# Optimization experiments

Hardware: AMD Instinct MI355X
Metric: run time of the kernel (lower is better)

The kernel has to match this reference:

```python
import jax, jax.numpy as jnp
import numpy as np

# T-MAC weight-only quantized linear, mathematically-equivalent reference.
# Weights: ternary {-1,0,1} via per-tensor scale s_w = 1/mean|W| (pesudo_tmac_weight_quant,
# force_per_tensor=True). Dequant scale = 1/s_w.
# Activations: the LUT preprocessing quantizes per act_group_size=64 group to uint8 with
# per-group LUT_Scales/LUT_Biases; equivalent math is symmetric int8 per-group quantization.
# qgemm_lut accumulates LUT entries indexed by weight bits == qW @ x_hat, then applies scales.

ACT_GROUP = 64  # op_config.act_group_size


def setup_inputs() -> dict:
    key = jax.random.key(0)
    k1, k2 = jax.random.split(key)
    N, M, K = 8, 8192, 8192
    x = jax.random.normal(k1, (N, K), dtype=jnp.float32)
    weight = jax.random.normal(k2, (M, K), dtype=jnp.float32) * 0.02
    return {"x": x, "weight": weight}


def reference(x, weight):
    M, K = weight.shape
    N = x.shape[0]
    # --- weight ternary quantization (per-tensor) ---
    s_w = 1.0 / jnp.clip(jnp.mean(jnp.abs(weight)), 1e-5, None)
    qW = jnp.clip(jnp.round(weight * s_w), -1.0, 1.0)  # [M, K] in {-1,0,1}
    w_deq = 1.0 / s_w  # per-tensor dequant scale (weight_scales)
    # --- activation per-group int8 quantization (LUT precision emulation) ---
    xg = x.reshape(N, K // ACT_GROUP, ACT_GROUP)
    a_scale = jnp.maximum(jnp.max(jnp.abs(xg), axis=-1, keepdims=True) / 127.0, 1e-8)
    x_hat = (jnp.round(xg / a_scale) * a_scale).reshape(N, K)
    # --- lookup-accumulate GEMM == dense GEMM with quantized operands ---
    y = jnp.einsum('nk,mk->nm', x_hat, qW) * w_deq  # [N, M]
    return y.astype(x.dtype)
```

## Files before the change

### kernel.cpp

```cpp
#include <hip/hip_runtime.h>
#include <math.h>

#define K_DIM 8192
#define M_DIM 8192
#define N_DIM 8
#define KC 1024
#define RED_BLOCKS 2048

__global__ __launch_bounds__(256) void k_abssum(const float4* __restrict__ W4,
                                                double* __restrict__ partials,
                                                int n4) {
    int tid = blockIdx.x * blockDim.x + threadIdx.x;
    int stride = gridDim.x * blockDim.x;
    float s0 = 0.f, s1 = 0.f, s2 = 0.f, s3 = 0.f;
    for (int i = tid; i < n4; i += stride) {
        float4 v = W4[i];
        s0 += fabsf(v.x); s1 += fabsf(v.y);
        s2 += fabsf(v.z); s3 += fabsf(v.w);
    }
    float s = (s0 + s1) + (s2 + s3);
    #pragma unroll
    for (int off = 32; off > 0; off >>= 1) s += __shfl_xor(s, off, 64);
    __shared__ float sm[4];
    if ((threadIdx.x & 63) == 0) sm[threadIdx.x >> 6] = s;
    __syncthreads();
    if (threadIdx.x == 0) {
        double t = ((double)sm[0] + (double)sm[1]) +
                   ((double)sm[2] + (double)sm[3]);
        partials[blockIdx.x] = t;
    }
}

__global__ __launch_bounds__(256) void k_final(const double* __restrict__ partials,
                                               int nparts,
                                               float* __restrict__ scal) {
    double s = 0.0;
    for (int i = threadIdx.x; i < nparts; i += 256) s += partials[i];
    #pragma unroll
    for (int off = 32; off > 0; off >>= 1) s += __shfl_xor(s, off, 64);
    __shared__ double sm[4];
    if ((threadIdx.x & 63) == 0) sm[threadIdx.x >> 6] = s;
    __syncthreads();
    if (threadIdx.x == 0) {
        double tot = (sm[0] + sm[1]) + (sm[2] + sm[3]);
        float meanf = (float)(tot / (double)((long long)M_DIM * K_DIM));
        float clipped = fmaxf(meanf, 1e-5f);
        float s_w = 1.0f / clipped;
        float w_deq = 1.0f / s_w;
        scal[0] = s_w;
        scal[1] = w_deq;
    }
}

__global__ __launch_bounds__(256) void k_actq(const float* __restrict__ x,
                                              float* __restrict__ xh) {
    int idx = blockIdx.x * blockDim.x + threadIdx.x;
    float v = x[idx];
    float a = fabsf(v);
    #pragma unroll
    for (int off = 32; off > 0; off >>= 1) a = fmaxf(a, __shfl_xor(a, off, 64));
    float scale = fmaxf(a / 127.0f, 1e-8f);
    float q = rintf(v / scale);
    xh[idx] = q * scale;
}

__device__ __forceinline__ float quant1(float w, float s_w) {
    return fminf(1.0f, fmaxf(-1.0f, rintf(w * s_w)));
}

__global__ __launch_bounds__(256) void k_gemm(const float* __restrict__ W,
                                              const float* __restrict__ xh,
                                              const float* __restrict__ scal,
                                              float* __restrict__ out) {
    __shared__ float lds[N_DIM * KC];
    const float s_w  = scal[0];
    const float w_deq = scal[1];
    const int wave = threadIdx.x >> 6;
    const int lane = threadIdx.x & 63;
    const int m0 = blockIdx.x * 16 + wave * 4;

    const float* Wr0 = W + (size_t)(m0 + 0) * K_DIM;
    const float* Wr1 = W + (size_t)(m0 + 1) * K_DIM;
    const float* Wr2 = W + (size_t)(m0 + 2) * K_DIM;
    const float* Wr3 = W + (size_t)(m0 + 3) * K_DIM;

    float acc[4][8];
    #pragma unroll
    for (int r = 0; r < 4; ++r)
        #pragma unroll
        for (int n = 0; n < 8; ++n) acc[r][n] = 0.0f;

    for (int c0 = 0; c0 < K_DIM; c0 += KC) {
        #pragma unroll
        for (int i = 0; i < 8; ++i) {
            int idx = threadIdx.x + i * 256;
            int n = idx >> 8;
            int kk4 = idx & 255;
            float4 v = *(const float4*)(xh + n * K_DIM + c0 + kk4 * 4);
            *(float4*)(lds + n * KC + kk4 * 4) = v;
        }
        __syncthreads();

        #pragma unroll
        for (int it = 0; it < KC / 256; ++it) {
            const int kk = it * 256 + lane * 4;
            const int k = c0 + kk;
            float4 w0 = *(const float4*)(Wr0 + k);
            float4 w1 = *(const float4*)(Wr1 + k);
            float4 w2 = *(const float4*)(Wr2 + k);
            float4 w3 = *(const float4*)(Wr3 + k);
            float4 xv[8];
            #pragma unroll
            for (int n = 0; n < 8; ++n)
                xv[n] = *(const float4*)(lds + n * KC + kk);

            float4 q0, q1, q2, q3;
            q0.x = quant1(w0.x, s_w); q0.y = quant1(w0.y, s_w);
            q0.z = quant1(w0.z, s_w); q0.w = quant1(w0.w, s_w);
            q1.x = quant1(w1.x, s_w); q1.y = quant1(w1.y, s_w);
            q1.z = quant1(w1.z, s_w); q1.w = quant1(w1.w, s_w);
            q2.x = quant1(w2.x, s_w); q2.y = quant1(w2.y, s_w);
            q2.z = quant1(w2.z, s_w); q2.w = quant1(w2.w, s_w);
            q3.x = quant1(w3.x, s_w); q3.y = quant1(w3.y, s_w);
            q3.z = quant1(w3.z, s_w); q3.w = quant1(w3.w, s_w);

            #pragma unroll
            for (int n = 0; n < 8; ++n) {
                acc[0][n] = fmaf(q0.x, xv[n].x, acc[0][n]);
                acc[0][n] = fmaf(q0.y, xv[n].y, acc[0][n]);
                acc[0][n] = fmaf(q0.z, xv[n].z, acc[0][n]);
                acc[0][n] = fmaf(q0.w, xv[n].w, acc[0][n]);
                acc[1][n] = fmaf(q1.x, xv[n].x, acc[1][n]);
                acc[1][n] = fmaf(q1.y, xv[n].y, acc[1][n]);
                acc[1][n] = fmaf(q1.z, xv[n].z, acc[1][n]);
                acc[1][n] = fmaf(q1.w, xv[n].w, acc[1][n]);
                acc[2][n] = fmaf(q2.x, xv[n].x, acc[2][n]);
                acc[2][n] = fmaf(q2.y, xv[n].y, acc[2][n]);
                acc[2][n] = fmaf(q2.z, xv[n].z, acc[2][n]);
                acc[2][n] = fmaf(q2.w, xv[n].w, acc[2][n]);
                acc[3][n] = fmaf(q3.x, xv[n].x, acc[3][n]);
                acc[3][n] = fmaf(q3.y, xv[n].y, acc[3][n]);
                acc[3][n] = fmaf(q3.z, xv[n].z, acc[3][n]);
                acc[3][n] = fmaf(q3.w, xv[n].w, acc[3][n]);
            }
        }
        __syncthreads();
    }

    #pragma unroll
    for (int r = 0; r < 4; ++r) {
        #pragma unroll
        for (int n = 0; n < 8; ++n) {
            float v = acc[r][n];
            #pragma unroll
            for (int off = 32; off > 0; off >>= 1) v += __shfl_xor(v, off, 64);
            acc[r][n] = v;
        }
    }
    if (lane == 0) {
        #pragma unroll
        for (int r = 0; r < 4; ++r)
            #pragma unroll
            for (int n = 0; n < 8; ++n)
                out[n * M_DIM + (m0 + r)] = w_deq * acc[r][n];
    }
}

extern "C" void kernel_launch(void* const* d_in, const int* in_sizes, int n_in,
                              void* d_out, int out_size, void* d_ws, size_t ws_size,
                              hipStream_t stream) {
    const float* x = (const float*)d_in[0];
    const float* W = (const float*)d_in[1];
    float* out = (float*)d_out;

    double* partials = (double*)d_ws;
    float* scal = (float*)((char*)d_ws + 16384);
    float* xh = (float*)((char*)d_ws + 32768);

    const int n4 = (M_DIM * K_DIM) / 4;

    k_abssum<<<RED_BLOCKS, 256, 0, stream>>>((const float4*)W, partials, n4);
    k_final<<<1, 256, 0, stream>>>(partials, RED_BLOCKS, scal);
    k_actq<<<(N_DIM * K_DIM) / 256, 256, 0, stream>>>(x, xh);
    k_gemm<<<M_DIM / 16, 256, 0, stream>>>(W, xh, scal, out);
}
```

Before: 412.1 us.

## Fuse reductions and activation quant into two kernels, drop LDS staging in GEMM

Merges the four launches into two. The first kernel computes per-block abs-sum partials over contiguous weight chunks and also quantizes the activations. The second kernel has every block redundantly reduce the partials to get the scale, then runs the GEMM reading activations straight from global/L2 instead of staging them in LDS with barriers. This removes two launches and the per-chunk syncs, at the cost of each of the 512 blocks repeating the partials reduction and leaning on cache for the activation reads.

```diff
diff --git a/kernel.cpp b/kernel.cpp
--- a/kernel.cpp
+++ b/kernel.cpp
@@ -4,17 +4,17 @@
 #define K_DIM 8192
 #define M_DIM 8192
 #define N_DIM 8
-#define KC 1024
 #define RED_BLOCKS 2048
 
-__global__ __launch_bounds__(256) void k_abssum(const float4* __restrict__ W4,
-                                                double* __restrict__ partials,
-                                                int n4) {
-    int tid = blockIdx.x * blockDim.x + threadIdx.x;
-    int stride = gridDim.x * blockDim.x;
+__global__ __launch_bounds__(256) void k_pass1(const float4* __restrict__ W4,
+                                               const float* __restrict__ x,
+                                               double* __restrict__ partials,
+                                               float* __restrict__ xh) {
+    const float4* p = W4 + (size_t)blockIdx.x * 8192 + threadIdx.x;
     float s0 = 0.f, s1 = 0.f, s2 = 0.f, s3 = 0.f;
-    for (int i = tid; i < n4; i += stride) {
-        float4 v = W4[i];
+    #pragma unroll 8
+    for (int j = 0; j < 32; ++j) {
+        float4 v = p[(size_t)j * 256];
         s0 += fabsf(v.x); s1 += fabsf(v.y);
         s2 += fabsf(v.z); s3 += fabsf(v.w);
     }
@@ -29,52 +29,41 @@
                    ((double)sm[2] + (double)sm[3]);
         partials[blockIdx.x] = t;
     }
-}
 
-__global__ __launch_bounds__(256) void k_final(const double* __restrict__ partials,
-                                               int nparts,
-                                               float* __restrict__ scal) {
-    double s = 0.0;
-    for (int i = threadIdx.x; i < nparts; i += 256) s += partials[i];
-    #pragma unroll
-    for (int off = 32; off > 0; off >>= 1) s += __shfl_xor(s, off, 64);
-    __shared__ double sm[4];
-    if ((threadIdx.x & 63) == 0) sm[threadIdx.x >> 6] = s;
-    __syncthreads();
-    if (threadIdx.x == 0) {
-        double tot = (sm[0] + sm[1]) + (sm[2] + sm[3]);
-        float meanf = (float)(tot / (double)((long long)M_DIM * K_DIM));
-        float clipped = fmaxf(meanf, 1e-5f);
-        float s_w = 1.0f / clipped;
-        float w_deq = 1.0f / s_w;
-        scal[0] = s_w;
-        scal[1] = w_deq;
+    if (blockIdx.x < (N_DIM * K_DIM) / 256) {
+        int idx = blockIdx.x * 256 + threadIdx.x;
+        float v = x[idx];
+        float a = fabsf(v);
+        #pragma unroll
+        for (int off = 32; off > 0; off >>= 1)
+            a = fmaxf(a, __shfl_xor(a, off, 64));
+        float scale = fmaxf(a / 127.0f, 1e-8f);
+        xh[idx] = rintf(v / scale) * scale;
     }
-}
-
-__global__ __launch_bounds__(256) void k_actq(const float* __restrict__ x,
-                                              float* __restrict__ xh) {
-    int idx = blockIdx.x * blockDim.x + threadIdx.x;
-    float v = x[idx];
-    float a = fabsf(v);
-    #pragma unroll
-    for (int off = 32; off > 0; off >>= 1) a = fmaxf(a, __shfl_xor(a, off, 64));
-    float scale = fmaxf(a / 127.0f, 1e-8f);
-    float q = rintf(v / scale);
-    xh[idx] = q * scale;
 }
 
 __device__ __forceinline__ float quant1(float w, float s_w) {
     return fminf(1.0f, fmaxf(-1.0f, rintf(w * s_w)));
 }
 
-__global__ __launch_bounds__(256) void k_gemm(const float* __restrict__ W,
-                                              const float* __restrict__ xh,
-                                              const float* __restrict__ scal,
-                                              float* __restrict__ out) {
-    __shared__ float lds[N_DIM * KC];
-    const float s_w  = scal[0];
-    const float w_deq = scal[1];
+__global__ __launch_bounds__(256) void k_pass2(const float* __restrict__ W,
+                                               const float* __restrict__ xh,
+                                               const double* __restrict__ partials,
+                                               float* __restrict__ out) {
+    double s = 0.0;
+    #pragma unroll
+    for (int j = 0; j < RED_BLOCKS / 256; ++j)
+        s += partials[threadIdx.x + j * 256];
+    #pragma unroll
+    for (int off = 32; off > 0; off >>= 1) s += __shfl_xor(s, off, 64);
+    __shared__ double sm[4];
+    if ((threadIdx.x & 63) == 0) sm[threadIdx.x >> 6] = s;
+    __syncthreads();
+    const double tot = (sm[0] + sm[1]) + (sm[2] + sm[3]);
+    const float meanf = (float)(tot / (double)((long long)M_DIM * K_DIM));
+    const float s_w = 1.0f / fmaxf(meanf, 1e-5f);
+    const float w_deq = 1.0f / s_w;
+
     const int wave = threadIdx.x >> 6;
     const int lane = threadIdx.x & 63;
     const int m0 = blockIdx.x * 16 + wave * 4;
@@ -90,61 +79,46 @@
         #pragma unroll
         for (int n = 0; n < 8; ++n) acc[r][n] = 0.0f;
 
-    for (int c0 = 0; c0 < K_DIM; c0 += KC) {
+    #pragma unroll 2
+    for (int k = lane * 4; k < K_DIM; k += 256) {
+        float4 w0 = *(const float4*)(Wr0 + k);
+        float4 w1 = *(const float4*)(Wr1 + k);
+        float4 w2 = *(const float4*)(Wr2 + k);
+        float4 w3 = *(const float4*)(Wr3 + k);
+        float4 xv[8];
         #pragma unroll
-        for (int i = 0; i < 8; ++i) {
-            int idx = threadIdx.x + i * 256;
-            int n = idx >> 8;
-            int kk4 = idx & 255;
-            float4 v = *(const float4*)(xh + n * K_DIM + c0 + kk4 * 4);
-            *(float4*)(lds + n * KC + kk4 * 4) = v;
-        }
-        __syncthreads();
+        for (int n = 0; n < 8; ++n)
+            xv[n] = *(const float4*)(xh + n * K_DIM + k);
+
+        float4 q0, q1, q2, q3;
+        q0.x = quant1(w0.x, s_w); q0.y = quant1(w0.y, s_w);
+        q0.z = quant1(w0.z, s_w); q0.w = quant1(w0.w, s_w);
+        q1.x = quant1(w1.x, s_w); q1.y = quant1(w1.y, s_w);
+        q1.z = quant1(w1.z, s_w); q1.w = quant1(w1.w, s_w);
+        q2.x = quant1(w2.x, s_w); q2.y = quant1(w2.y, s_w);
+        q2.z = quant1(w2.z, s_w); q2.w = quant1(w2.w, s_w);
+        q3.x = quant1(w3.x, s_w); q3.y = quant1(w3.y, s_w);
+        q3.z = quant1(w3.z, s_w); q3.w = quant1(w3.w, s_w);
 
         #pragma unroll
-        for (int it = 0; it < KC / 256; ++it) {
-            const int kk = it * 256 + lane * 4;
-            const int k = c0 + kk;
-            float4 w0 = *(const float4*)(Wr0 + k);
-            float4 w1 = *(const float4*)(Wr1 + k);
-            float4 w2 = *(const float4*)(Wr2 + k);
-            float4 w3 = *(const float4*)(Wr3 + k);
-            float4 xv[8];
-            #pragma unroll
-            for (int n = 0; n < 8; ++n)
-                xv[n] = *(const float4*)(lds + n * KC + kk);
-
-            float4 q0, q1, q2, q3;
-            q0.x = quant1(w0.x, s_w); q0.y = quant1(w0.y, s_w);
-            q0.z = quant1(w0.z, s_w); q0.w = quant1(w0.w, s_w);
-            q1.x = quant1(w1.x, s_w); q1.y = quant1(w1.y, s_w);
-            q1.z = quant1(w1.z, s_w); q1.w = quant1(w1.w, s_w);
-            q2.x = quant1(w2.x, s_w); q2.y = quant1(w2.y, s_w);
-            q2.z = quant1(w2.z, s_w); q2.w = quant1(w2.w, s_w);
-            q3.x = quant1(w3.x, s_w); q3.y = quant1(w3.y, s_w);
-            q3.z = quant1(w3.z, s_w); q3.w = quant1(w3.w, s_w);
-
-            #pragma unroll
-            for (int n = 0; n < 8; ++n) {
-                acc[0][n] = fmaf(q0.x, xv[n].x, acc[0][n]);
-                acc[0][n] = fmaf(q0.y, xv[n].y, acc[0][n]);
-                acc[0][n] = fmaf(q0.z, xv[n].z, acc[0][n]);
-                acc[0][n] = fmaf(q0.w, xv[n].w, acc[0][n]);
-                acc[1][n] = fmaf(q1.x, xv[n].x, acc[1][n]);
-                acc[1][n] = fmaf(q1.y, xv[n].y, acc[1][n]);
-                acc[1][n] = fmaf(q1.z, xv[n].z, acc[1][n]);
-                acc[1][n] = fmaf(q1.w, xv[n].w, acc[1][n]);
-                acc[2][n] = fmaf(q2.x, xv[n].x, acc[2][n]);
-                acc[2][n] = fmaf(q2.y, xv[n].y, acc[2][n]);
-                acc[2][n] = fmaf(q2.z, xv[n].z, acc[2][n]);
-                acc[2][n] = fmaf(q2.w, xv[n].w, acc[2][n]);
-                acc[3][n] = fmaf(q3.x, xv[n].x, acc[3][n]);
-                acc[3][n] = fmaf(q3.y, xv[n].y, acc[3][n]);
-                acc[3][n] = fmaf(q3.z, xv[n].z, acc[3][n]);
-                acc[3][n] = fmaf(q3.w, xv[n].w, acc[3][n]);
-            }
+        for (int n = 0; n < 8; ++n) {
+            acc[0][n] = fmaf(q0.x, xv[n].x, acc[0][n]);
+            acc[0][n] = fmaf(q0.y, xv[n].y, acc[0][n]);
+            acc[0][n] = fmaf(q0.z, xv[n].z, acc[0][n]);
+            acc[0][n] = fmaf(q0.w, xv[n].w, acc[0][n]);
+            acc[1][n] = fmaf(q1.x, xv[n].x, acc[1][n]);
+            acc[1][n] = fmaf(q1.y, xv[n].y, acc[1][n]);
+            acc[1][n] = fmaf(q1.z, xv[n].z, acc[1][n]);
+            acc[1][n] = fmaf(q1.w, xv[n].w, acc[1][n]);
+            acc[2][n] = fmaf(q2.x, xv[n].x, acc[2][n]);
+            acc[2][n] = fmaf(q2.y, xv[n].y, acc[2][n]);
+            acc[2][n] = fmaf(q2.z, xv[n].z, acc[2][n]);
+            acc[2][n] = fmaf(q2.w, xv[n].w, acc[2][n]);
+            acc[3][n] = fmaf(q3.x, xv[n].x, acc[3][n]);
+            acc[3][n] = fmaf(q3.y, xv[n].y, acc[3][n]);
+            acc[3][n] = fmaf(q3.z, xv[n].z, acc[3][n]);
+            acc[3][n] = fmaf(q3.w, xv[n].w, acc[3][n]);
         }
-        __syncthreads();
     }
 
     #pragma unroll
@@ -174,13 +148,8 @@
     float* out = (float*)d_out;
 
     double* partials = (double*)d_ws;
-    float* scal = (float*)((char*)d_ws + 16384);
     float* xh = (float*)((char*)d_ws + 32768);
 
-    const int n4 = (M_DIM * K_DIM) / 4;
-
-    k_abssum<<<RED_BLOCKS, 256, 0, stream>>>((const float4*)W, partials, n4);
-    k_final<<<1, 256, 0, stream>>>(partials, RED_BLOCKS, scal);
-    k_actq<<<(N_DIM * K_DIM) / 256, 256, 0, stream>>>(x, xh);
-    k_gemm<<<M_DIM / 16, 256, 0, stream>>>(W, xh, scal, out);
+    k_pass1<<<RED_BLOCKS, 256, 0, stream>>>((const float4*)W, x, partials, xh);
+    k_pass2<<<M_DIM / 16, 256, 0, stream>>>(W, xh, partials, out);
 }
```

Measured after the change: 429.9 us. +4.3%, slower.
